# Kernel optimization log

Hardware: AMD Instinct MI355X
Metric: run time of the kernel (lower is better)

The kernel has to match this reference:

```python
import jax, jax.numpy as jnp
import numpy as np

EMBED_DIM = 1024
NUM_HEADS = 16
HEAD_DIM = EMBED_DIM // NUM_HEADS


def setup_inputs() -> dict:
    key = jax.random.key(0)
    k_x, k_wqkv, k_bqkv, k_wo, k_bo = jax.random.split(key, 5)
    B, T, C = 8, 1024, EMBED_DIM
    s = 1.0 / np.sqrt(C)
    return {
        "x": jax.random.normal(k_x, (B, T, C), dtype=jnp.float32),
        "W_qkv": jax.random.uniform(k_wqkv, (C, 3 * C), minval=-s, maxval=s, dtype=jnp.float32),
        "b_qkv": jax.random.uniform(k_bqkv, (3 * C,), minval=-s, maxval=s, dtype=jnp.float32),
        "W_out": jax.random.uniform(k_wo, (C, C), minval=-s, maxval=s, dtype=jnp.float32),
        "b_out": jax.random.uniform(k_bo, (C,), minval=-s, maxval=s, dtype=jnp.float32),
    }


def reference(x, W_qkv, b_qkv, W_out, b_out):
    B, T, C = x.shape
    H, D = NUM_HEADS, HEAD_DIM
    qkv = x @ W_qkv + b_qkv                      # [B,T,3C]
    q, k, v = jnp.split(qkv, 3, axis=-1)
    q = q.reshape(B, T, H, D).transpose(0, 2, 1, 3)  # [B,H,T,D]
    k = k.reshape(B, T, H, D).transpose(0, 2, 1, 3)
    v = v.reshape(B, T, H, D).transpose(0, 2, 1, 3)
    scores = jnp.einsum("bhqd,bhkd->bhqk", q, k) / np.sqrt(D).astype(np.float32)
    causal = jnp.tril(jnp.ones((T, T), dtype=bool))
    scores = jnp.where(causal[None, None], scores, -jnp.inf)
    attn = jax.nn.softmax(scores, axis=-1)       # dropout is identity in eval
    out = jnp.einsum("bhqk,bhkd->bhqd", attn, v)
    out = out.transpose(0, 2, 1, 3).reshape(B, T, C)
    return out @ W_out + b_out
```

## Files before the change

kernel.cpp:

```cpp
#include <hip/hip_runtime.h>
#include <hip/hip_bf16.h>
#include <cstdint>

using bf16 = __hip_bfloat16;
typedef short short8 __attribute__((ext_vector_type(8)));
typedef float floatx4 __attribute__((ext_vector_type(4)));

#define QSCALE 0.1803368801111601f

__device__ __forceinline__ void async_load16(const bf16* g, bf16* l) {
    __builtin_amdgcn_global_load_lds(
        (const __attribute__((address_space(1))) uint32_t*)g,
        (__attribute__((address_space(3))) uint32_t*)l, 16, 0, 0);
}

__device__ __forceinline__ void bar_lgkm0() {
    asm volatile("s_waitcnt lgkmcnt(0)\ns_barrier" ::: "memory");
}
__device__ __forceinline__ void bar_vm4() {
    asm volatile("s_waitcnt vmcnt(4)\ns_barrier" ::: "memory");
}
__device__ __forceinline__ void bar_vm0() {
    asm volatile("s_waitcnt vmcnt(0)\ns_barrier" ::: "memory");
}
__device__ __forceinline__ void bar_vm0_lgkm0() {
    asm volatile("s_waitcnt vmcnt(0) lgkmcnt(0)\ns_barrier" ::: "memory");
}

__device__ __forceinline__ uint32_t pack2(float a, float b) {
    union { bf16 h[2]; uint32_t u; } p;
    p.h[0] = __float2bfloat16(a);
    p.h[1] = __float2bfloat16(b);
    return p.u;
}

__global__ __launch_bounds__(256)
void cvt_bf16_kernel(const float* __restrict__ in, bf16* __restrict__ out) {
    const int i = (blockIdx.x * 256 + threadIdx.x) * 4;
    const float4 v = *(const float4*)(in + i);
    bf16 o[4] = {__float2bfloat16(v.x), __float2bfloat16(v.y),
                 __float2bfloat16(v.z), __float2bfloat16(v.w)};
    *(ushort4*)(out + i) = *(ushort4*)o;
}

__global__ __launch_bounds__(256)
void transpose_cvt2_kernel(const float* __restrict__ inA, bf16* __restrict__ outA,
                           const float* __restrict__ inB, bf16* __restrict__ outB) {
    __shared__ float tile[32][33];
    const int tx = threadIdx.x & 31, ty = threadIdx.x >> 5;
    const bool isB = blockIdx.x >= 96;
    const float* __restrict__ in = isB ? inB : inA;
    bf16* __restrict__ out = isB ? outB : outA;
    const int C = isB ? 1024 : 3072;
    const int bx = isB ? blockIdx.x - 96 : blockIdx.x;
    const int c0 = bx * 32, r0 = blockIdx.y * 32;
    const int R = 1024;
    #pragma unroll
    for (int i = 0; i < 32; i += 8)
        tile[ty + i][tx] = in[(size_t)(r0 + ty + i) * C + c0 + tx];
    __syncthreads();
    #pragma unroll
    for (int i = 0; i < 32; i += 8)
        out[(size_t)(c0 + ty + i) * R + r0 + tx] = __float2bfloat16(tile[tx][ty + i]);
}

template <int MODE>
__global__ __launch_bounds__(256, 5)
void gemm_bt_kernel(const bf16* __restrict__ A, const bf16* __restrict__ Bt,
                    const float* __restrict__ bias, int K,
                    bf16* __restrict__ q_ws, bf16* __restrict__ k_ws,
                    bf16* __restrict__ vt_ws, float* __restrict__ out, int N) {
    __shared__ bf16 As[2][128 * 32];
    __shared__ bf16 Bs[2][128 * 32];
    const int tid = threadIdx.x;
    const int wave = tid >> 6, lane = tid & 63;
    const int ln = lane & 15, quad = lane >> 4;
    const int wm = wave & 1, wn = wave >> 1;
    const int m0 = blockIdx.y * 128, n0 = blockIdx.x * 128;

    floatx4 acc[4][4] = {};
    const int nkt = K >> 5;

    #pragma unroll
    for (int c = 0; c < 2; ++c) {
        const int e = (c * 256 + tid) * 8;
        const int row = e >> 5;
        const int gch = ((((e >> 3) & 3) ^ ((row >> 1) & 3)) << 3);
        async_load16(A + (size_t)(m0 + row) * K + gch,
                     &As[0][(c * 256 + wave * 64) * 8]);
    }
    #pragma unroll
    for (int c = 0; c < 2; ++c) {
        const int e = (c * 256 + tid) * 8;
        const int row = e >> 5;
        const int gch = ((((e >> 3) & 3) ^ ((row >> 1) & 3)) << 3);
        async_load16(Bt + (size_t)(n0 + row) * K + gch,
                     &Bs[0][(c * 256 + wave * 64) * 8]);
    }

    for (int kt = 0; kt < nkt; ++kt) {
        const int cur = kt & 1;
        bar_vm0_lgkm0();

        if (kt + 1 < nkt) {
            const int k0 = (kt + 1) << 5;
            #pragma unroll
            for (int c = 0; c < 2; ++c) {
                const int e = (c * 256 + tid) * 8;
                const int row = e >> 5;
                const int gch = ((((e >> 3) & 3) ^ ((row >> 1) & 3)) << 3);
                async_load16(A + (size_t)(m0 + row) * K + k0 + gch,
                             &As[cur ^ 1][(c * 256 + wave * 64) * 8]);
            }
            #pragma unroll
            for (int c = 0; c < 2; ++c) {
                const int e = (c * 256 + tid) * 8;
                const int row = e >> 5;
                const int gch = ((((e >> 3) & 3) ^ ((row >> 1) & 3)) << 3);
                async_load16(Bt + (size_t)(n0 + row) * K + k0 + gch,
                             &Bs[cur ^ 1][(c * 256 + wave * 64) * 8]);
            }
        }

        const int chq = ((quad ^ ((ln >> 1) & 3)) << 3);
        short8 af[4], bfr[4];
        #pragma unroll
        for (int i = 0; i < 4; ++i) {
            af[i]  = *(const short8*)&As[cur][(wm * 64 + i * 16 + ln) * 32 + chq];
            bfr[i] = *(const short8*)&Bs[cur][(wn * 64 + i * 16 + ln) * 32 + chq];
        }
        #pragma unroll
        for (int mi = 0; mi < 4; ++mi)
            #pragma unroll
            for (int ni = 0; ni < 4; ++ni)
                acc[mi][ni] = __builtin_amdgcn_mfma_f32_16x16x32_bf16(
                    af[mi], bfr[ni], acc[mi][ni], 0, 0, 0);
    }

    #pragma unroll
    for (int ni = 0; ni < 4; ++ni) {
        const int col = n0 + wn * 64 + ni * 16 + ln;
        const float bv = bias[col];
        if (MODE == 0) {
            const int which = col >> 10;
            const int cc = col & 1023;
            const int h = cc >> 6, d = cc & 63;
            #pragma unroll
            for (int mi = 0; mi < 4; ++mi) {
                const int rowb = m0 + wm * 64 + mi * 16 + quad * 4;
                if (which == 2) {
                    const int bb = rowb >> 10, t = rowb & 1023;
                    const int tl = t & 63;
                    const int tt = (t & ~63) + ((((tl >> 3) ^ (d & 7)) << 3) | (tl & 7));
                    uint2 w2 = { pack2(acc[mi][ni][0] + bv, acc[mi][ni][1] + bv),
                                 pack2(acc[mi][ni][2] + bv, acc[mi][ni][3] + bv) };
                    *(uint2*)&vt_ws[((size_t)(bb * 16 + h) * 64 + d) * 1024 + tt] = w2;
                } else {
                    bf16* dst = (which == 0) ? q_ws : k_ws;
                    #pragma unroll
                    for (int r = 0; r < 4; ++r) {
                        const int row = rowb + r;
                        const int bb = row >> 10, t = row & 1023;
                        float v = acc[mi][ni][r] + bv;
                        if (which == 0) v *= QSCALE;
                        const int dd = (((d >> 3) ^ (t & 7)) << 3) | (d & 7);
                        dst[((size_t)(bb * 16 + h) * 1024 + t) * 64 + dd] =
                            __float2bfloat16(v);
                    }
                }
            }
        } else {
            #pragma unroll
            for (int mi = 0; mi < 4; ++mi) {
                const int rowb = m0 + wm * 64 + mi * 16 + quad * 4;
                #pragma unroll
                for (int r = 0; r < 4; ++r)
                    out[(size_t)(rowb + r) * N + col] = acc[mi][ni][r] + bv;
            }
        }
    }
}

__global__ __launch_bounds__(256, 4)
void attn_kernel(const bf16* __restrict__ Q, const bf16* __restrict__ K,
                 const bf16* __restrict__ Vt, bf16* __restrict__ O) {
    constexpr int T = 1024;
    __shared__ bf16 QPs[64 * 64];
    __shared__ bf16 Ks[2][64 * 64];
    __shared__ bf16 Vts[2][64 * 64];

    const int bh = blockIdx.y;
    const int tid = threadIdx.x;
    const int wave = tid >> 6, lane = tid & 63;
    const int ln = lane & 15, quad = lane >> 4;

    const bf16* Kg = K + (size_t)bh * T * 64;
    const bf16* Vg = Vt + (size_t)bh * 64 * T;
    const int b = bh >> 4, h = bh & 15;

    #pragma unroll
    for (int phase = 0; phase < 2; ++phase) {
        const int jt = phase ? 15 - blockIdx.x : blockIdx.x;
        const int q0 = jt * 64;
        const int nkt = jt + 1;

        bar_lgkm0();

        const bf16* Qg = Q + (size_t)bh * T * 64 + (size_t)q0 * 64;
        #pragma unroll
        for (int c = 0; c < 2; ++c)
            async_load16(Qg + (size_t)(c * 256 + tid) * 8,
                         &QPs[(c * 256 + wave * 64) * 8]);
        #pragma unroll
        for (int c = 0; c < 2; ++c)
            async_load16(Kg + (size_t)(c * 256 + tid) * 8,
                         &Ks[0][(c * 256 + wave * 64) * 8]);
        #pragma unroll
        for (int c = 0; c < 2; ++c) {
            const int e = (c * 256 + tid) * 8;
            async_load16(Vg + (size_t)(e >> 6) * T + (e & 63),
                         &Vts[0][(c * 256 + wave * 64) * 8]);
        }
        bar_vm0();

        short8 bq[2];
        #pragma unroll
        for (int ks = 0; ks < 2; ++ks) {
            const int row = wave * 16 + ln;
            const int ch = (ks * 4 + quad) ^ (row & 7);
            bq[ks] = *(const short8*)&QPs[row * 64 + ch * 8];
        }

        floatx4 oacc[4] = {};
        float rl = 0.f;
        const int qbw = q0 + wave * 16;

        for (int kt = 0; kt < nkt; ++kt) {
            const int cur = kt & 1;
            bar_lgkm0();
            if (kt + 1 < nkt) {
                const int nxt = cur ^ 1;
                #pragma unroll
                for (int c = 0; c < 2; ++c)
                    async_load16(Kg + (size_t)(kt + 1) * 4096 + (size_t)(c * 256 + tid) * 8,
                                 &Ks[nxt][(c * 256 + wave * 64) * 8]);
                #pragma unroll
                for (int c = 0; c < 2; ++c) {
                    const int e = (c * 256 + tid) * 8;
                    async_load16(Vg + (size_t)(e >> 6) * T + (kt + 1) * 64 + (e & 63),
                                 &Vts[nxt][(c * 256 + wave * 64) * 8]);
                }
                bar_vm4();
            } else {
                bar_vm0();
            }

            const int k0 = kt * 64;
            if (k0 > qbw + 15) continue;
            const bool tail = (k0 + 63 > qbw);

            floatx4 sacc[4] = {};
            #pragma unroll
            for (int nj = 0; nj < 4; ++nj) {
                if (tail && k0 + nj * 16 > qbw + 15) continue;
                #pragma unroll
                for (int ks = 0; ks < 2; ++ks) {
                    const int row = nj * 16 + ln;
                    const int ch = (ks * 4 + quad) ^ (row & 7);
                    const short8 ak = *(const short8*)&Ks[cur][row * 64 + ch * 8];
                    sacc[nj] = __builtin_amdgcn_mfma_f32_16x16x32_bf16(
                        ak, bq[ks], sacc[nj], 0, 0, 0);
                }
            }

            if (tail) {
                const int qq = qbw + ln;
                #pragma unroll
                for (int nj = 0; nj < 4; ++nj)
                    #pragma unroll
                    for (int r = 0; r < 4; ++r) {
                        const int kk = k0 + nj * 16 + quad * 4 + r;
                        if (kk > qq) sacc[nj][r] = -1e30f;
                    }
            }

            {
                float rs = 0.f;
                const int qrow = wave * 16 + ln;
                #pragma unroll
                for (int nj = 0; nj < 4; ++nj) {
                    float p[4];
                    #pragma unroll
                    for (int r = 0; r < 4; ++r) {
                        p[r] = exp2f(sacc[nj][r]);
                        rs += p[r];
                    }
                    const int kcol = nj * 16 + quad * 4;
                    const int ch = (kcol >> 3) ^ (qrow & 7);
                    uint2 w2 = { pack2(p[0], p[1]), pack2(p[2], p[3]) };
                    *(uint2*)&QPs[qrow * 64 + ch * 8 + (kcol & 7)] = w2;
                }
                rl += rs;
            }

            #pragma unroll
            for (int ks4 = 0; ks4 < 2; ++ks4) {
                const int qrow = wave * 16 + ln;
                const int chp = (ks4 * 4 + quad) ^ (qrow & 7);
                const short8 bp = *(const short8*)&QPs[qrow * 64 + chp * 8];
                #pragma unroll
                for (int dt = 0; dt < 4; ++dt) {
                    const int row = dt * 16 + ln;
                    const int ch = (ks4 * 4 + quad) ^ (row & 7);
                    const short8 av = *(const short8*)&Vts[cur][row * 64 + ch * 8];
                    oacc[dt] = __builtin_amdgcn_mfma_f32_16x16x32_bf16(
                        av, bp, oacc[dt], 0, 0, 0);
                }
            }
        }

        {
            float l = rl;
            l += __shfl_xor(l, 16, 64);
            l += __shfl_xor(l, 32, 64);
            const float inv = 1.0f / l;
            const int t = q0 + wave * 16 + ln;
            const size_t rowb = ((size_t)b * 1024 + t) * 1024 + h * 64;
            #pragma unroll
            for (int dt = 0; dt < 4; ++dt) {
                uint2 w2 = { pack2(oacc[dt][0] * inv, oacc[dt][1] * inv),
                             pack2(oacc[dt][2] * inv, oacc[dt][3] * inv) };
                *(uint2*)&O[rowb + dt * 16 + quad * 4] = w2;
            }
        }
    }
}

extern "C" void kernel_launch(void* const* d_in, const int* in_sizes, int n_in,
                              void* d_out, int out_size, void* d_ws, size_t ws_size,
                              hipStream_t stream) {
    const float* x     = (const float*)d_in[0];
    const float* W_qkv = (const float*)d_in[1];
    const float* b_qkv = (const float*)d_in[2];
    const float* W_out = (const float*)d_in[3];
    const float* b_out = (const float*)d_in[4];
    float* out = (float*)d_out;

    char* ws = (char*)d_ws;
    const size_t MB = 1u << 20;
    bf16* x_bf   = (bf16*)(ws + 0);
    bf16* wqkv_t = (bf16*)(ws + 16 * MB);
    bf16* wout_t = (bf16*)(ws + 22 * MB);
    bf16* q_ws   = (bf16*)(ws + 24 * MB);
    bf16* k_ws   = (bf16*)(ws + 40 * MB);
    bf16* vt_ws  = (bf16*)(ws + 56 * MB);
    bf16* ao_ws  = (bf16*)(ws + 72 * MB);

    cvt_bf16_kernel<<<8192, 256, 0, stream>>>(x, x_bf);
    transpose_cvt2_kernel<<<dim3(128, 32), 256, 0, stream>>>(W_qkv, wqkv_t, W_out, wout_t);

    gemm_bt_kernel<0><<<dim3(24, 64), 256, 0, stream>>>(
        x_bf, wqkv_t, b_qkv, 1024, q_ws, k_ws, vt_ws, nullptr, 3072);

    attn_kernel<<<dim3(8, 128), 256, 0, stream>>>(q_ws, k_ws, vt_ws, ao_ws);

    gemm_bt_kernel<1><<<dim3(8, 64), 256, 0, stream>>>(
        ao_ws, wout_t, b_out, 1024, nullptr, nullptr, nullptr, out, 1024);
}
```

Before: 280.7 us.

## Triple-buffer GEMM loads and widen attention query tile to 128 rows

The GEMM kernel moves from double to triple buffering, prefetching two K-tiles ahead and waiting with vmcnt(4), which should hide more global-load latency. Its occupancy hint drops from 5 to 3 blocks. The attention kernel gives up the paired-phase scheme in which each block handled two 64-row query tiles one after the other. Each block now handles a single 128-row query tile, so every K/V tile loaded into LDS feeds twice as many MFMAs, and s_setprio is raised around the MFMA sections. The price is more registers and LDS per block and lower occupancy. Work is also less balanced across blocks, since blocks now range from 2 to 16 K/V tiles instead of getting balanced paired tiles.

```diff
diff --git a/kernel.cpp b/kernel.cpp
--- a/kernel.cpp
+++ b/kernel.cpp
@@ -22,6 +22,9 @@
 }
 __device__ __forceinline__ void bar_vm0() {
     asm volatile("s_waitcnt vmcnt(0)\ns_barrier" ::: "memory");
+}
+__device__ __forceinline__ void bar_vm4_lgkm0() {
+    asm volatile("s_waitcnt vmcnt(4) lgkmcnt(0)\ns_barrier" ::: "memory");
 }
 __device__ __forceinline__ void bar_vm0_lgkm0() {
     asm volatile("s_waitcnt vmcnt(0) lgkmcnt(0)\ns_barrier" ::: "memory");
@@ -65,13 +68,13 @@
 }
 
 template <int MODE>
-__global__ __launch_bounds__(256, 5)
+__global__ __launch_bounds__(256, 3)
 void gemm_bt_kernel(const bf16* __restrict__ A, const bf16* __restrict__ Bt,
                     const float* __restrict__ bias, int K,
                     bf16* __restrict__ q_ws, bf16* __restrict__ k_ws,
                     bf16* __restrict__ vt_ws, float* __restrict__ out, int N) {
-    __shared__ bf16 As[2][128 * 32];
-    __shared__ bf16 Bs[2][128 * 32];
+    __shared__ bf16 As[3][128 * 32];
+    __shared__ bf16 Bs[3][128 * 32];
     const int tid = threadIdx.x;
     const int wave = tid >> 6, lane = tid & 63;
     const int ln = lane & 15, quad = lane >> 4;
@@ -82,35 +85,41 @@
     const int nkt = K >> 5;
 
     #pragma unroll
-    for (int c = 0; c < 2; ++c) {
-        const int e = (c * 256 + tid) * 8;
-        const int row = e >> 5;
-        const int gch = ((((e >> 3) & 3) ^ ((row >> 1) & 3)) << 3);
-        async_load16(A + (size_t)(m0 + row) * K + gch,
-                     &As[0][(c * 256 + wave * 64) * 8]);
-    }
-    #pragma unroll
-    for (int c = 0; c < 2; ++c) {
-        const int e = (c * 256 + tid) * 8;
-        const int row = e >> 5;
-        const int gch = ((((e >> 3) & 3) ^ ((row >> 1) & 3)) << 3);
-        async_load16(Bt + (size_t)(n0 + row) * K + gch,
-                     &Bs[0][(c * 256 + wave * 64) * 8]);
+    for (int t = 0; t < 2; ++t) {
+        const int k0 = t << 5;
+        #pragma unroll
+        for (int c = 0; c < 2; ++c) {
+            const int e = (c * 256 + tid) * 8;
+            const int row = e >> 5;
+            const int gch = ((((e >> 3) & 3) ^ ((row >> 1) & 3)) << 3);
+            async_load16(A + (size_t)(m0 + row) * K + k0 + gch,
+                         &As[t][(c * 256 + wave * 64) * 8]);
+        }
+        #pragma unroll
+        for (int c = 0; c < 2; ++c) {
+            const int e = (c * 256 + tid) * 8;
+            const int row = e >> 5;
+            const int gch = ((((e >> 3) & 3) ^ ((row >> 1) & 3)) << 3);
+            async_load16(Bt + (size_t)(n0 + row) * K + k0 + gch,
+                         &Bs[t][(c * 256 + wave * 64) * 8]);
+        }
     }
 
     for (int kt = 0; kt < nkt; ++kt) {
-        const int cur = kt & 1;
-        bar_vm0_lgkm0();
-
-        if (kt + 1 < nkt) {
-            const int k0 = (kt + 1) << 5;
+        const int cur = kt % 3;
+        if (kt + 1 < nkt) bar_vm4_lgkm0();
+        else              bar_vm0_lgkm0();
+
+        if (kt + 2 < nkt) {
+            const int nxt = (kt + 2) % 3;
+            const int k0 = (kt + 2) << 5;
             #pragma unroll
             for (int c = 0; c < 2; ++c) {
                 const int e = (c * 256 + tid) * 8;
                 const int row = e >> 5;
                 const int gch = ((((e >> 3) & 3) ^ ((row >> 1) & 3)) << 3);
                 async_load16(A + (size_t)(m0 + row) * K + k0 + gch,
-                             &As[cur ^ 1][(c * 256 + wave * 64) * 8]);
+                             &As[nxt][(c * 256 + wave * 64) * 8]);
             }
             #pragma unroll
             for (int c = 0; c < 2; ++c) {
@@ -118,7 +127,7 @@
                 const int row = e >> 5;
                 const int gch = ((((e >> 3) & 3) ^ ((row >> 1) & 3)) << 3);
                 async_load16(Bt + (size_t)(n0 + row) * K + k0 + gch,
-                             &Bs[cur ^ 1][(c * 256 + wave * 64) * 8]);
+                             &Bs[nxt][(c * 256 + wave * 64) * 8]);
             }
         }
 
@@ -181,11 +190,11 @@
     }
 }
 
-__global__ __launch_bounds__(256, 4)
+__global__ __launch_bounds__(256, 3)
 void attn_kernel(const bf16* __restrict__ Q, const bf16* __restrict__ K,
                  const bf16* __restrict__ Vt, bf16* __restrict__ O) {
     constexpr int T = 1024;
-    __shared__ bf16 QPs[64 * 64];
+    __shared__ bf16 QPs[128 * 64];
     __shared__ bf16 Ks[2][64 * 64];
     __shared__ bf16 Vts[2][64 * 64];
 
@@ -198,140 +207,160 @@
     const bf16* Vg = Vt + (size_t)bh * 64 * T;
     const int b = bh >> 4, h = bh & 15;
 
-    #pragma unroll
-    for (int phase = 0; phase < 2; ++phase) {
-        const int jt = phase ? 15 - blockIdx.x : blockIdx.x;
-        const int q0 = jt * 64;
-        const int nkt = jt + 1;
-
+    const int jt = 7 - blockIdx.x;
+    const int q0 = jt * 128;
+    const int nkt = 2 * jt + 2;
+
+    const bf16* Qg = Q + (size_t)bh * T * 64 + (size_t)q0 * 64;
+    #pragma unroll
+    for (int c = 0; c < 4; ++c)
+        async_load16(Qg + (size_t)(c * 256 + tid) * 8,
+                     &QPs[(c * 256 + wave * 64) * 8]);
+    #pragma unroll
+    for (int c = 0; c < 2; ++c)
+        async_load16(Kg + (size_t)(c * 256 + tid) * 8,
+                     &Ks[0][(c * 256 + wave * 64) * 8]);
+    #pragma unroll
+    for (int c = 0; c < 2; ++c) {
+        const int e = (c * 256 + tid) * 8;
+        async_load16(Vg + (size_t)(e >> 6) * T + (e & 63),
+                     &Vts[0][(c * 256 + wave * 64) * 8]);
+    }
+    bar_vm0();
+
+    short8 bq[2][2];
+    #pragma unroll
+    for (int qs = 0; qs < 2; ++qs)
+        #pragma unroll
+        for (int ks = 0; ks < 2; ++ks) {
+            const int row = wave * 16 + qs * 64 + ln;
+            const int ch = (ks * 4 + quad) ^ (row & 7);
+            bq[qs][ks] = *(const short8*)&QPs[row * 64 + ch * 8];
+        }
+
+    floatx4 oacc[2][4] = {};
+    float rl[2] = {0.f, 0.f};
+    const int qb0 = q0 + wave * 16;
+    const int qb1 = qb0 + 64;
+
+    for (int kt = 0; kt < nkt; ++kt) {
+        const int cur = kt & 1;
         bar_lgkm0();
-
-        const bf16* Qg = Q + (size_t)bh * T * 64 + (size_t)q0 * 64;
-        #pragma unroll
-        for (int c = 0; c < 2; ++c)
-            async_load16(Qg + (size_t)(c * 256 + tid) * 8,
-                         &QPs[(c * 256 + wave * 64) * 8]);
-        #pragma unroll
-        for (int c = 0; c < 2; ++c)
-            async_load16(Kg + (size_t)(c * 256 + tid) * 8,
-                         &Ks[0][(c * 256 + wave * 64) * 8]);
-        #pragma unroll
-        for (int c = 0; c < 2; ++c) {
-            const int e = (c * 256 + tid) * 8;
-            async_load16(Vg + (size_t)(e >> 6) * T + (e & 63),
-                         &Vts[0][(c * 256 + wave * 64) * 8]);
-        }
-        bar_vm0();
-
-        short8 bq[2];
-        #pragma unroll
-        for (int ks = 0; ks < 2; ++ks) {
-            const int row = wave * 16 + ln;
-            const int ch = (ks * 4 + quad) ^ (row & 7);
-            bq[ks] = *(const short8*)&QPs[row * 64 + ch * 8];
-        }
-
-        floatx4 oacc[4] = {};
-        float rl = 0.f;
-        const int qbw = q0 + wave * 16;
-
-        for (int kt = 0; kt < nkt; ++kt) {
-            const int cur = kt & 1;
-            bar_lgkm0();
-            if (kt + 1 < nkt) {
-                const int nxt = cur ^ 1;
-                #pragma unroll
-                for (int c = 0; c < 2; ++c)
-                    async_load16(Kg + (size_t)(kt + 1) * 4096 + (size_t)(c * 256 + tid) * 8,
-                                 &Ks[nxt][(c * 256 + wave * 64) * 8]);
-                #pragma unroll
-                for (int c = 0; c < 2; ++c) {
-                    const int e = (c * 256 + tid) * 8;
-                    async_load16(Vg + (size_t)(e >> 6) * T + (kt + 1) * 64 + (e & 63),
-                                 &Vts[nxt][(c * 256 + wave * 64) * 8]);
-                }
-                bar_vm4();
-            } else {
-                bar_vm0();
-            }
-
-            const int k0 = kt * 64;
-            if (k0 > qbw + 15) continue;
-            const bool tail = (k0 + 63 > qbw);
-
-            floatx4 sacc[4] = {};
-            #pragma unroll
-            for (int nj = 0; nj < 4; ++nj) {
-                if (tail && k0 + nj * 16 > qbw + 15) continue;
-                #pragma unroll
-                for (int ks = 0; ks < 2; ++ks) {
-                    const int row = nj * 16 + ln;
-                    const int ch = (ks * 4 + quad) ^ (row & 7);
-                    const short8 ak = *(const short8*)&Ks[cur][row * 64 + ch * 8];
-                    sacc[nj] = __builtin_amdgcn_mfma_f32_16x16x32_bf16(
-                        ak, bq[ks], sacc[nj], 0, 0, 0);
-                }
-            }
-
-            if (tail) {
-                const int qq = qbw + ln;
+        if (kt + 1 < nkt) {
+            const int nxt = cur ^ 1;
+            #pragma unroll
+            for (int c = 0; c < 2; ++c)
+                async_load16(Kg + (size_t)(kt + 1) * 4096 + (size_t)(c * 256 + tid) * 8,
+                             &Ks[nxt][(c * 256 + wave * 64) * 8]);
+            #pragma unroll
+            for (int c = 0; c < 2; ++c) {
+                const int e = (c * 256 + tid) * 8;
+                async_load16(Vg + (size_t)(e >> 6) * T + (kt + 1) * 64 + (e & 63),
+                             &Vts[nxt][(c * 256 + wave * 64) * 8]);
+            }
+            bar_vm4();
+        } else {
+            bar_vm0();
+        }
+
+        const int k0 = kt * 64;
+        if (k0 > qb1 + 15) continue;
+        const bool tail = (k0 + 63 > qb0);
+
+        floatx4 sacc[2][4] = {};
+        __builtin_amdgcn_s_setprio(1);
+        #pragma unroll
+        for (int nj = 0; nj < 4; ++nj) {
+            short8 ak[2];
+            #pragma unroll
+            for (int ks = 0; ks < 2; ++ks) {
+                const int row = nj * 16 + ln;
+                const int ch = (ks * 4 + quad) ^ (row & 7);
+                ak[ks] = *(const short8*)&Ks[cur][row * 64 + ch * 8];
+            }
+            #pragma unroll
+            for (int qs = 0; qs < 2; ++qs) {
+                const int qb = qs ? qb1 : qb0;
+                if (k0 + nj * 16 > qb + 15) continue;
+                #pragma unroll
+                for (int ks = 0; ks < 2; ++ks)
+                    sacc[qs][nj] = __builtin_amdgcn_mfma_f32_16x16x32_bf16(
+                        ak[ks], bq[qs][ks], sacc[qs][nj], 0, 0, 0);
+            }
+        }
+        __builtin_amdgcn_s_setprio(0);
+
+        if (tail) {
+            #pragma unroll
+            for (int qs = 0; qs < 2; ++qs) {
+                const int qq = (qs ? qb1 : qb0) + ln;
                 #pragma unroll
                 for (int nj = 0; nj < 4; ++nj)
                     #pragma unroll
                     for (int r = 0; r < 4; ++r) {
                         const int kk = k0 + nj * 16 + quad * 4 + r;
-                        if (kk > qq) sacc[nj][r] = -1e30f;
+                        if (kk > qq) sacc[qs][nj][r] = -1e30f;
                     }
             }
-
-            {
-                float rs = 0.f;
-                const int qrow = wave * 16 + ln;
-                #pragma unroll
-                for (int nj = 0; nj < 4; ++nj) {
-                    float p[4];
-                    #pragma unroll
-                    for (int r = 0; r < 4; ++r) {
-                        p[r] = exp2f(sacc[nj][r]);
-                        rs += p[r];
-                    }
-                    const int kcol = nj * 16 + quad * 4;
-                    const int ch = (kcol >> 3) ^ (qrow & 7);
-                    uint2 w2 = { pack2(p[0], p[1]), pack2(p[2], p[3]) };
-                    *(uint2*)&QPs[qrow * 64 + ch * 8 + (kcol & 7)] = w2;
+        }
+
+        #pragma unroll
+        for (int qs = 0; qs < 2; ++qs) {
+            float rs = 0.f;
+            const int qrow = wave * 16 + qs * 64 + ln;
+            #pragma unroll
+            for (int nj = 0; nj < 4; ++nj) {
+                float p[4];
+                #pragma unroll
+                for (int r = 0; r < 4; ++r) {
+                    p[r] = exp2f(sacc[qs][nj][r]);
+                    rs += p[r];
                 }
-                rl += rs;
-            }
-
-            #pragma unroll
-            for (int ks4 = 0; ks4 < 2; ++ks4) {
-                const int qrow = wave * 16 + ln;
+                const int kcol = nj * 16 + quad * 4;
+                const int ch = (kcol >> 3) ^ (qrow & 7);
+                uint2 w2 = { pack2(p[0], p[1]), pack2(p[2], p[3]) };
+                *(uint2*)&QPs[qrow * 64 + ch * 8 + (kcol & 7)] = w2;
+            }
+            rl[qs] += rs;
+        }
+
+        __builtin_amdgcn_s_setprio(1);
+        #pragma unroll
+        for (int ks4 = 0; ks4 < 2; ++ks4) {
+            short8 bp[2];
+            #pragma unroll
+            for (int qs = 0; qs < 2; ++qs) {
+                const int qrow = wave * 16 + qs * 64 + ln;
                 const int chp = (ks4 * 4 + quad) ^ (qrow & 7);
-                const short8 bp = *(const short8*)&QPs[qrow * 64 + chp * 8];
-                #pragma unroll
-                for (int dt = 0; dt < 4; ++dt) {
-                    const int row = dt * 16 + ln;
-                    const int ch = (ks4 * 4 + quad) ^ (row & 7);
-                    const short8 av = *(const short8*)&Vts[cur][row * 64 + ch * 8];
-                    oacc[dt] = __builtin_amdgcn_mfma_f32_16x16x32_bf16(
-                        av, bp, oacc[dt], 0, 0, 0);
-                }
-            }
-        }
-
-        {
-            float l = rl;
-            l += __shfl_xor(l, 16, 64);
-            l += __shfl_xor(l, 32, 64);
-            const float inv = 1.0f / l;
-            const int t = q0 + wave * 16 + ln;
-            const size_t rowb = ((size_t)b * 1024 + t) * 1024 + h * 64;
+                bp[qs] = *(const short8*)&QPs[qrow * 64 + chp * 8];
+            }
             #pragma unroll
             for (int dt = 0; dt < 4; ++dt) {
-                uint2 w2 = { pack2(oacc[dt][0] * inv, oacc[dt][1] * inv),
-                             pack2(oacc[dt][2] * inv, oacc[dt][3] * inv) };
-                *(uint2*)&O[rowb + dt * 16 + quad * 4] = w2;
-            }
+                const int row = dt * 16 + ln;
+                const int ch = (ks4 * 4 + quad) ^ (row & 7);
+                const short8 av = *(const short8*)&Vts[cur][row * 64 + ch * 8];
+                #pragma unroll
+                for (int qs = 0; qs < 2; ++qs)
+                    oacc[qs][dt] = __builtin_amdgcn_mfma_f32_16x16x32_bf16(
+                        av, bp[qs], oacc[qs][dt], 0, 0, 0);
+            }
+        }
+        __builtin_amdgcn_s_setprio(0);
+    }
+
+    #pragma unroll
+    for (int qs = 0; qs < 2; ++qs) {
+        float l = rl[qs];
+        l += __shfl_xor(l, 16, 64);
+        l += __shfl_xor(l, 32, 64);
+        const float inv = 1.0f / l;
+        const int t = q0 + qs * 64 + wave * 16 + ln;
+        const size_t rowb = ((size_t)b * 1024 + t) * 1024 + h * 64;
+        #pragma unroll
+        for (int dt = 0; dt < 4; ++dt) {
+            uint2 w2 = { pack2(oacc[qs][dt][0] * inv, oacc[qs][dt][1] * inv),
+                         pack2(oacc[qs][dt][2] * inv, oacc[qs][dt][3] * inv) };
+            *(uint2*)&O[rowb + dt * 16 + quad * 4] = w2;
         }
     }
 }
```

Result: faster. 267.5 us (-4.7%).
